# Kernel tuning notes

Measured on AMD Instinct MI355X. Metric: run time of the kernel, lower is better.

## Reference

```python
import jax, jax.numpy as jnp
import numpy as np

K_HEADS, D_HEAD = 8, 8
D = K_HEADS * D_HEAD  # 64


def _fc(x, W, b=None, relu=False):
    # 1x1 Conv2D over (B,T,N,C) == per-position dense
    y = x @ W
    if b is not None:
        y = y + b
    return jax.nn.relu(y) if relu else y


def _split_heads(x):
    # (B,T,N,K*d) -> (K,B,T,N,d); matches torch.cat(torch.split(x, d, -1), 0)
    B, T, N, _ = x.shape
    return x.reshape(B, T, N, K_HEADS, D_HEAD).transpose(3, 0, 1, 2, 4)


def _merge_heads(x):
    # (K,B,T,N,d) -> (B,T,N,K*d); matches torch.cat(torch.split(x, B, 0), -1)
    K, B, T, N, d = x.shape
    return x.transpose(1, 2, 3, 0, 4).reshape(B, T, N, K * d)


def _forward(X, TLE, key_padding_mask, *P):
    (sa_Wq, sa_bq, sa_Wk, sa_bk, sa_Wv, sa_bv, sa_Wo1, sa_bo1, sa_Wo2, sa_bo2,
     ta_Wq, ta_bq, ta_Wk, ta_bk, ta_Wv, ta_bv, ta_Wo1, ta_bo1, ta_Wo2, ta_bo2,
     g_Wxs, g_Wxt, g_bxt, g_Wh1, g_bh1, g_Wh2, g_bh2) = P
    B, T, N, _ = X.shape
    scale = 1.0 / (D_HEAD ** 0.5)
    XE = jnp.concatenate([X, TLE], axis=-1)  # (B,T,N,3D)

    # ---- Spatial attention (over nodes) ----
    q = _split_heads(_fc(XE, sa_Wq, sa_bq, True))
    k = _split_heads(_fc(XE, sa_Wk, sa_bk, True))
    v = _split_heads(_fc(XE, sa_Wv, sa_bv, True))
    s = jnp.einsum('kbtnd,kbtmd->kbtnm', q, k) * scale  # (K,B,T,N,N)
    p = jax.nn.softmax(s, axis=-1)
    HS = _merge_heads(jnp.einsum('kbtnm,kbtmd->kbtnd', p, v))
    HS = _fc(_fc(HS, sa_Wo1, sa_bo1, True), sa_Wo2, sa_bo2)

    # ---- Temporal attention (over time, causal + key padding) ----
    q = _split_heads(_fc(XE, ta_Wq, ta_bq, True))
    k = _split_heads(_fc(XE, ta_Wk, ta_bk, True))
    v = _split_heads(_fc(XE, ta_Wv, ta_bv, True))
    s = jnp.einsum('kbind,kbjnd->kbnij', q, k) * scale  # (K,B,N,T,T)
    causal = jnp.tril(jnp.ones((T, T), dtype=bool))  # (T,T)
    valid_key = jnp.arange(T)[None, :] < key_padding_mask  # (B,T)
    m = causal[None, None, None] & valid_key[None, :, None, None, :]
    s = jnp.where(m, s, -jnp.inf)
    p = jax.nn.softmax(s, axis=-1)
    HT = _merge_heads(jnp.einsum('kbnij,kbjnd->kbind', p, v))
    HT = _fc(_fc(HT, ta_Wo1, ta_bo1, True), ta_Wo2, ta_bo2)

    # ---- Gated fusion + residual ----
    z = jax.nn.sigmoid(HS @ g_Wxs + HT @ g_Wxt + g_bxt)
    H = z * HS + (1.0 - z) * HT
    H = _fc(_fc(H, g_Wh1, g_bh1, True), g_Wh2, g_bh2)
    return X + H


_PARAM_SHAPES = []
for _pre in ('sa', 'ta'):
    _PARAM_SHAPES += [(_pre + '_Wq', (3 * D, D)), (_pre + '_bq', (D,)),
                      (_pre + '_Wk', (3 * D, D)), (_pre + '_bk', (D,)),
                      (_pre + '_Wv', (3 * D, D)), (_pre + '_bv', (D,)),
                      (_pre + '_Wo1', (D, D)), (_pre + '_bo1', (D,)),
                      (_pre + '_Wo2', (D, D)), (_pre + '_bo2', (D,))]
_PARAM_SHAPES += [('g_Wxs', (D, D)), ('g_Wxt', (D, D)), ('g_bxt', (D,)),
                  ('g_Wh1', (D, D)), ('g_bh1', (D,)),
                  ('g_Wh2', (D, D)), ('g_bh2', (D,))]


def setup_inputs() -> dict:
    key = jax.random.key(0)
    ks = jax.random.split(key, 3 + len(_PARAM_SHAPES))
    B, T, N = 16, 24, 128
    inp = {
        'X': jax.random.normal(ks[0], (B, T, N, D), dtype=jnp.float32),
        'TLE': jax.random.normal(ks[1], (B, T, N, 2 * D), dtype=jnp.float32),
        'key_padding_mask': jax.random.randint(ks[2], (B, 1), 1, T + 1),
    }
    for i, (nm, shp) in enumerate(_PARAM_SHAPES):
        inp[nm] = jax.random.normal(ks[3 + i], shp, dtype=jnp.float32) * 0.05
    return inp


def reference(X, TLE, key_padding_mask,
              sa_Wq, sa_bq, sa_Wk, sa_bk, sa_Wv, sa_bv, sa_Wo1, sa_bo1, sa_Wo2, sa_bo2,
              ta_Wq, ta_bq, ta_Wk, ta_bk, ta_Wv, ta_bv, ta_Wo1, ta_bo1, ta_Wo2, ta_bo2,
              g_Wxs, g_Wxt, g_bxt, g_Wh1, g_bh1, g_Wh2, g_bh2):
    return _forward(X, TLE, key_padding_mask,
                    sa_Wq, sa_bq, sa_Wk, sa_bk, sa_Wv, sa_bv, sa_Wo1, sa_bo1, sa_Wo2, sa_bo2,
                    ta_Wq, ta_bq, ta_Wk, ta_bk, ta_Wv, ta_bv, ta_Wo1, ta_bo1, ta_Wo2, ta_bo2,
                    g_Wxs, g_Wxt, g_bxt, g_Wh1, g_bh1, g_Wh2, g_bh2)
```

## Files before the change

kernel.cpp:

```cpp
#include <hip/hip_runtime.h>
#include <math.h>

#define BB 16
#define TT 24
#define NN 128
#define DD 64
#define PTOT (BB * TT * NN)
#define P64  (PTOT * 64)

typedef __attribute__((ext_vector_type(8))) short bf16x8;
typedef __attribute__((ext_vector_type(4))) float f32x4;
typedef __attribute__((ext_vector_type(16))) float f32x16;

__device__ __forceinline__ unsigned short f2bf(float f) {
    unsigned u = __builtin_bit_cast(unsigned, f);
    u = (u + 0x7fffu + ((u >> 16) & 1u)) >> 16;
    return (unsigned short)u;
}
__device__ __forceinline__ unsigned cvt_pk_bf16(float a, float b) {
    unsigned r;
    asm("v_cvt_pk_bf16_f32 %0, %1, %2" : "=v"(r) : "v"(a), "v"(b));
    return r;
}
__device__ __forceinline__ void unpack8(uint4 u, float* f) {
    f[0] = __builtin_bit_cast(float, u.x << 16);
    f[1] = __builtin_bit_cast(float, u.x & 0xFFFF0000u);
    f[2] = __builtin_bit_cast(float, u.y << 16);
    f[3] = __builtin_bit_cast(float, u.y & 0xFFFF0000u);
    f[4] = __builtin_bit_cast(float, u.z << 16);
    f[5] = __builtin_bit_cast(float, u.z & 0xFFFF0000u);
    f[6] = __builtin_bit_cast(float, u.w << 16);
    f[7] = __builtin_bit_cast(float, u.w & 0xFFFF0000u);
}
__device__ __forceinline__ uint4 pack8(const float* f) {
    uint4 o;
    o.x = cvt_pk_bf16(f[0], f[1]);
    o.y = cvt_pk_bf16(f[2], f[3]);
    o.z = cvt_pk_bf16(f[4], f[5]);
    o.w = cvt_pk_bf16(f[6], f[7]);
    return o;
}
__device__ __forceinline__ float fast_exp2(float x) {
#if __has_builtin(__builtin_amdgcn_exp2f)
    return __builtin_amdgcn_exp2f(x);
#else
    return exp2f(x);
#endif
}
__device__ __forceinline__ f32x16 zero16() {
    f32x16 z;
    #pragma unroll
    for (int i = 0; i < 16; ++i) z[i] = 0.f;
    return z;
}

__global__ __launch_bounds__(256) void wprep_all(
    const float* __restrict__ W0, const float* __restrict__ W1,
    const float* __restrict__ W2, const float* __restrict__ W3,
    const float* __restrict__ W4, const float* __restrict__ W5,
    const float* __restrict__ E0, const float* __restrict__ E1,
    const float* __restrict__ E2, const float* __restrict__ E3,
    const float* __restrict__ E4, const float* __restrict__ E5,
    const float* __restrict__ E6, const float* __restrict__ E7,
    unsigned short* __restrict__ Wt, unsigned short* __restrict__ Wt8)
{
    const int bid = blockIdx.x;
    if (bid < 288) {
        const float* Ws[6] = {W0, W1, W2, W3, W4, W5};
        const int e = bid * 256 + threadIdx.x;
        const int j = e / 12288;
        const int r = e % 12288;
        const int k = r / 64;
        const int n = r % 64;
        Wt[j * 12288 + n * 192 + k] = f2bf(Ws[j][k * 64 + n]);
    } else {
        const float* Es[8] = {E0, E1, E2, E3, E4, E5, E6, E7};
        const int e = (bid - 288) * 256 + threadIdx.x;
        const int mat = e >> 12;
        const int r = e & 4095;
        const int k = r >> 6;
        const int n = r & 63;
        Wt8[mat * 4096 + n * 64 + k] = f2bf(Es[mat][k * 64 + n]);
    }
}

__global__ __launch_bounds__(512, 4) void fused_sattn(
    const float* __restrict__ X, const float* __restrict__ TLE,
    const unsigned short* __restrict__ Wt,
    const float* __restrict__ b0, const float* __restrict__ b1,
    const float* __restrict__ b2, const float* __restrict__ b3,
    const float* __restrict__ b4, const float* __restrict__ b5,
    unsigned short* __restrict__ qt, unsigned short* __restrict__ kt,
    unsigned short* __restrict__ vt,
    unsigned short* __restrict__ HS)
{
    __shared__ __align__(16) unsigned short xe[2][16][200];
    __shared__ __align__(16) unsigned short qq[128 * 64];
    __shared__ __align__(16) unsigned short kk[128 * 64];
    __shared__ __align__(16) unsigned short vv[128 * 64];
    const int tid = threadIdx.x;
    const long p0 = (long)blockIdx.x * 128;
    const int w = tid >> 6, l = tid & 63, quad = l >> 4, l16 = l & 15;
    const int nt = w >> 1;
    const int mg = (w & 1) * 3;

    auto stage = [&](int mt, int buf) {
        #pragma unroll
        for (int i = 0; i < 2; ++i) {
            const int idx4 = tid + i * 512;
            if (idx4 < 768) {
                const int m  = idx4 / 48;
                const int kq = idx4 % 48;
                const int k  = kq * 4;
                const long p = p0 + mt * 16 + m;
                float4 v;
                if (k < 64) v = *reinterpret_cast<const float4*>(X + p * 64 + k);
                else        v = *reinterpret_cast<const float4*>(TLE + p * 128 + (k - 64));
                uint2 u;
                u.x = cvt_pk_bf16(v.x, v.y);
                u.y = cvt_pk_bf16(v.z, v.w);
                *reinterpret_cast<uint2*>(&xe[buf][m][k]) = u;
            }
        }
    };

    bf16x8 wf[3][6];
    #pragma unroll
    for (int mi = 0; mi < 3; ++mi)
        #pragma unroll
        for (int kc = 0; kc < 6; ++kc)
            wf[mi][kc] = *reinterpret_cast<const bf16x8*>(
                &Wt[(mg + mi) * 12288 + (nt * 16 + l16) * 192 + kc * 32 + quad * 8]);

    const float* bias_p[6] = {b0, b1, b2, b3, b4, b5};
    float4 bias[3];
    #pragma unroll
    for (int mi = 0; mi < 3; ++mi)
        bias[mi] = *reinterpret_cast<const float4*>(&bias_p[mg + mi][nt * 16 + quad * 4]);

    stage(0, 0);
    __syncthreads();

    const int chBase = nt * 16 + quad * 4;
    const int chunkW = nt * 2 + (quad >> 1);
    const int chSub  = (quad & 1) * 4;
    const float cs = 0.35355339059327373f * 1.4426950408889634f;

    for (int mt = 0; mt < 8; ++mt) {
        if (mt < 7) stage(mt + 1, (mt + 1) & 1);

        bf16x8 A[6];
        #pragma unroll
        for (int kc = 0; kc < 6; ++kc)
            A[kc] = *reinterpret_cast<const bf16x8*>(
                &xe[mt & 1][l16][kc * 32 + quad * 8]);

        f32x4 acc[3];
        #pragma unroll
        for (int mi = 0; mi < 3; ++mi)
            acc[mi] = (f32x4){bias[mi].x, bias[mi].y, bias[mi].z, bias[mi].w};
        #pragma unroll
        for (int kc = 0; kc < 6; ++kc)
            #pragma unroll
            for (int mi = 0; mi < 3; ++mi)
                acc[mi] = __builtin_amdgcn_mfma_f32_16x16x32_bf16(
                    wf[mi][kc], A[kc], acc[mi], 0, 0, 0);

        const int pos = mt * 16 + l16;
        if (mg == 0) {
            const int sw = pos * 64 + ((chunkW ^ (pos & 7)) << 3) + chSub;
            uint2 uq;
            uq.x = cvt_pk_bf16(fmaxf(acc[0][0], 0.f) * cs, fmaxf(acc[0][1], 0.f) * cs);
            uq.y = cvt_pk_bf16(fmaxf(acc[0][2], 0.f) * cs, fmaxf(acc[0][3], 0.f) * cs);
            *reinterpret_cast<uint2*>(&qq[sw]) = uq;
            uint2 uk;
            uk.x = cvt_pk_bf16(fmaxf(acc[1][0], 0.f), fmaxf(acc[1][1], 0.f));
            uk.y = cvt_pk_bf16(fmaxf(acc[1][2], 0.f), fmaxf(acc[1][3], 0.f));
            *reinterpret_cast<uint2*>(&kk[sw]) = uk;
            uint2 uv;
            uv.x = cvt_pk_bf16(fmaxf(acc[2][0], 0.f), fmaxf(acc[2][1], 0.f));
            uv.y = cvt_pk_bf16(fmaxf(acc[2][2], 0.f), fmaxf(acc[2][3], 0.f));
            *reinterpret_cast<uint2*>(&vv[sw]) = uv;
        } else {
            unsigned short* dstT[3] = {qt, kt, vt};
            const long gp = (p0 + pos) * 64 + chBase;
            #pragma unroll
            for (int mi = 0; mi < 3; ++mi) {
                uint2 u;
                u.x = cvt_pk_bf16(fmaxf(acc[mi][0], 0.f), fmaxf(acc[mi][1], 0.f));
                u.y = cvt_pk_bf16(fmaxf(acc[mi][2], 0.f), fmaxf(acc[mi][3], 0.f));
                *reinterpret_cast<uint2*>(&dstT[mi][gp]) = u;
            }
        }
        __builtin_amdgcn_sched_barrier(0);
        asm volatile("s_waitcnt lgkmcnt(0)" ::: "memory");
        __builtin_amdgcn_s_barrier();
        __builtin_amdgcn_sched_barrier(0);
    }

    const int h  = w;
    const int hi = l >> 5;
    const int ln = l & 31;
    bf16x8 zf = {};
    const int swz = (h ^ (ln & 7)) << 3;

    auto pvstep = [&](f32x16& st, const bf16x8& va0, const bf16x8& va1,
                      f32x16& oacc) {
        const unsigned P0 = cvt_pk_bf16(st[0],  st[1]);
        const unsigned P1 = cvt_pk_bf16(st[2],  st[3]);
        const unsigned P2 = cvt_pk_bf16(st[4],  st[5]);
        const unsigned P3 = cvt_pk_bf16(st[6],  st[7]);
        const unsigned P4 = cvt_pk_bf16(st[8],  st[9]);
        const unsigned P5 = cvt_pk_bf16(st[10], st[11]);
        const unsigned P6 = cvt_pk_bf16(st[12], st[13]);
        const unsigned P7 = cvt_pk_bf16(st[14], st[15]);
        const unsigned V0 = __shfl_xor(hi ? P0 : P2, 32);
        const unsigned V1 = __shfl_xor(hi ? P1 : P3, 32);
        const unsigned V2 = __shfl_xor(hi ? P4 : P6, 32);
        const unsigned V3 = __shfl_xor(hi ? P5 : P7, 32);
        uint4 fe, fo;
        fe.x = hi ? V0 : P0; fe.y = hi ? V1 : P1;
        fe.z = hi ? P2 : V0; fe.w = hi ? P3 : V1;
        fo.x = hi ? V2 : P4; fo.y = hi ? V3 : P5;
        fo.z = hi ? P6 : V2; fo.w = hi ? P7 : V3;
        oacc = __builtin_amdgcn_mfma_f32_32x32x16_bf16(
            va0, __builtin_bit_cast(bf16x8, fe), oacc, 0, 0, 0);
        oacc = __builtin_amdgcn_mfma_f32_32x32x16_bf16(
            va1, __builtin_bit_cast(bf16x8, fo), oacc, 0, 0, 0);
    };

    bf16x8 kf[4];
    #pragma unroll
    for (int t = 0; t < 4; ++t)
        kf[t] = hi ? zf : *reinterpret_cast<const bf16x8*>(&kk[(t * 32 + ln) * 64 + swz]);

    bf16x8 vf[8];
    #pragma unroll
    for (int c = 0; c < 8; ++c) {
        bf16x8 f = zf;
        if (ln < 8) {
            #pragma unroll
            for (int j = 0; j < 8; ++j) {
                const int m = c * 16 + hi * 8 + j;
                f[j] = (short)vv[m * 64 + ((h ^ (m & 7)) << 3) + ln];
            }
        }
        vf[c] = f;
    }

    #pragma unroll
    for (int ntq = 0; ntq < 4; ++ntq) {
        const int qrow = ntq * 32 + ln;
        bf16x8 qf = hi ? zf : *reinterpret_cast<const bf16x8*>(&qq[qrow * 64 + swz]);

        float sum = 0.f;
        f32x16 oacc = zero16();
        #pragma unroll
        for (int t = 0; t < 4; ++t) {
            f32x16 st = zero16();
            st = __builtin_amdgcn_mfma_f32_32x32x16_bf16(kf[t], qf, st, 0, 0, 0);
            #pragma unroll
            for (int r = 0; r < 16; ++r) { st[r] = fast_exp2(st[r]); sum += st[r]; }
            pvstep(st, vf[2 * t], vf[2 * t + 1], oacc);
        }
        sum += __shfl_xor(sum, 32);

        const float inv = 1.0f / sum;
        uint2 u;
        u.x = cvt_pk_bf16(oacc[0] * inv, oacc[1] * inv);
        u.y = cvt_pk_bf16(oacc[2] * inv, oacc[3] * inv);
        *reinterpret_cast<uint2*>(&HS[(p0 + qrow) * 64 + h * 8 + hi * 4]) = u;
    }
}

__global__ __launch_bounds__(192) void tattn_kernel(
    const unsigned short* __restrict__ Q, const unsigned short* __restrict__ Kb,
    const unsigned short* __restrict__ V, const int* __restrict__ kpm,
    unsigned short* __restrict__ O)
{
    __shared__ float kk[8][TT][8];
    __shared__ float vv[8][TT][8];
    const int tid = threadIdx.x;
    const int n = blockIdx.x & (NN - 1);
    const int b = blockIdx.x >> 7;

    {
        const int hs = tid / TT;
        const int j  = tid % TT;
        const long g = (((long)(b * TT + j)) * NN + n) * 64 + hs * 8;
        uint4 ku = *reinterpret_cast<const uint4*>(&Kb[g]);
        uint4 vu = *reinterpret_cast<const uint4*>(&V[g]);
        float kf[8], vf[8];
        unpack8(ku, kf); unpack8(vu, vf);
        #pragma unroll
        for (int d = 0; d < 8; ++d) { kk[hs][j][d] = kf[d]; vv[hs][j][d] = vf[d]; }
    }

    const int h = tid / TT;
    const int i = tid % TT;
    const long qb = (((long)(b * TT + i)) * NN + n) * 64 + h * 8;
    float q[8];
    {
        uint4 qu = *reinterpret_cast<const uint4*>(&Q[qb]);
        unpack8(qu, q);
    }
    __syncthreads();

    const int kp = kpm[b];
    const float scale = 0.35355339059327373f;

    float s[TT];
    #pragma unroll
    for (int j = 0; j < TT; ++j) {
        float t = 0.0f;
        #pragma unroll
        for (int d = 0; d < 8; ++d) t = fmaf(q[d], kk[h][j][d], t);
        s[j] = (j <= i && j < kp) ? t * scale : -INFINITY;
    }
    float mx = -INFINITY;
    #pragma unroll
    for (int j = 0; j < TT; ++j) mx = fmaxf(mx, s[j]);

    float sum = 0.0f;
    float acc[8];
    #pragma unroll
    for (int d = 0; d < 8; ++d) acc[d] = 0.0f;
    #pragma unroll
    for (int j = 0; j < TT; ++j) {
        const float e = __expf(s[j] - mx);
        sum += e;
        #pragma unroll
        for (int d = 0; d < 8; ++d) acc[d] = fmaf(e, vv[h][j][d], acc[d]);
    }
    const float inv = 1.0f / sum;
    float o[8];
    #pragma unroll
    for (int d = 0; d < 8; ++d) o[d] = acc[d] * inv;
    *reinterpret_cast<uint4*>(&O[qb]) = pack8(o);
}

__global__ __launch_bounds__(256) void epi_kernel(
    const float* __restrict__ X,
    const unsigned short* __restrict__ HSb, const unsigned short* __restrict__ HTb,
    const unsigned short* __restrict__ Wt8,
    const float* __restrict__ sbo1, const float* __restrict__ sbo2,
    const float* __restrict__ tbo1, const float* __restrict__ tbo2,
    const float* __restrict__ bxt,
    const float* __restrict__ bh1, const float* __restrict__ bh2,
    float* __restrict__ out)
{
    constexpr int RS = 72;
    __shared__ __align__(16) unsigned short bufA[64][RS], bufB[64][RS];
    __shared__ __align__(16) unsigned short bufC[64][RS], bufD[64][RS];
    const int tid = threadIdx.x;
    const long p0 = (long)blockIdx.x * 64;
    const int w = tid >> 6, l = tid & 63, quad = l >> 4, l16 = l & 15;
    const int chBase = w * 16 + quad * 4;

    #pragma unroll
    for (int i = 0; i < 4; ++i) {
        const int idx = tid + i * 256;
        const int m = idx >> 4;
        const int c = (idx & 15) * 4;
        *reinterpret_cast<ushort4*>(&bufA[m][c]) =
            *reinterpret_cast<const ushort4*>(&HSb[(p0 + m) * 64 + c]);
        *reinterpret_cast<ushort4*>(&bufC[m][c]) =
            *reinterpret_cast<const ushort4*>(&HTb[(p0 + m) * 64 + c]);
    }
    __syncthreads();

    auto gemm = [&](const unsigned short (*in)[RS], int mat,
                    const float* __restrict__ bias, f32x4* accO) {
        bf16x8 af[2];
        #pragma unroll
        for (int kc = 0; kc < 2; ++kc)
            af[kc] = *reinterpret_cast<const bf16x8*>(
                &Wt8[mat * 4096 + (w * 16 + l16) * 64 + kc * 32 + quad * 8]);
        const float4 b4 = *reinterpret_cast<const float4*>(&bias[chBase]);
        #pragma unroll
        for (int pt = 0; pt < 4; ++pt) {
            f32x4 acc = (f32x4){b4.x, b4.y, b4.z, b4.w};
            #pragma unroll
            for (int kc = 0; kc < 2; ++kc) {
                bf16x8 bf = *reinterpret_cast<const bf16x8*>(
                    &in[pt * 16 + l16][kc * 32 + quad * 8]);
                acc = __builtin_amdgcn_mfma_f32_16x16x32_bf16(af[kc], bf, acc, 0, 0, 0);
            }
            accO[pt] = acc;
        }
    };

    auto writeBuf = [&](unsigned short (*dst)[RS], const f32x4* v, bool relu) {
        #pragma unroll
        for (int pt = 0; pt < 4; ++pt) {
            float a0 = v[pt][0], a1 = v[pt][1], a2 = v[pt][2], a3 = v[pt][3];
            if (relu) { a0 = fmaxf(a0, 0.f); a1 = fmaxf(a1, 0.f);
                        a2 = fmaxf(a2, 0.f); a3 = fmaxf(a3, 0.f); }
            uint2 u;
            u.x = cvt_pk_bf16(a0, a1);
            u.y = cvt_pk_bf16(a2, a3);
            *reinterpret_cast<uint2*>(&dst[pt * 16 + l16][chBase]) = u;
        }
    };

    f32x4 tS[4], tT[4], HSr[4], HTr[4];

    gemm(bufA, 0, sbo1, tS);
    gemm(bufC, 2, tbo1, tT);
    __syncthreads();
    writeBuf(bufB, tS, true);
    writeBuf(bufD, tT, true);
    __syncthreads();

    gemm(bufB, 1, sbo2, HSr);
    gemm(bufD, 3, tbo2, HTr);
    __syncthreads();
    writeBuf(bufA, HSr, false);
    writeBuf(bufC, HTr, false);
    __syncthreads();

    {
        bf16x8 afS[2], afT[2];
        #pragma unroll
        for (int kc = 0; kc < 2; ++kc) {
            afS[kc] = *reinterpret_cast<const bf16x8*>(
                &Wt8[4 * 4096 + (w * 16 + l16) * 64 + kc * 32 + quad * 8]);
            afT[kc] = *reinterpret_cast<const bf16x8*>(
                &Wt8[5 * 4096 + (w * 16 + l16) * 64 + kc * 32 + quad * 8]);
        }
        const float4 b4 = *reinterpret_cast<const float4*>(&bxt[chBase]);
        #pragma unroll
        for (int pt = 0; pt < 4; ++pt) {
            f32x4 acc = (f32x4){b4.x, b4.y, b4.z, b4.w};
            #pragma unroll
            for (int kc = 0; kc < 2; ++kc) {
                bf16x8 hsf = *reinterpret_cast<const bf16x8*>(
                    &bufA[pt * 16 + l16][kc * 32 + quad * 8]);
                acc = __builtin_amdgcn_mfma_f32_16x16x32_bf16(afS[kc], hsf, acc, 0, 0, 0);
            }
            #pragma unroll
            for (int kc = 0; kc < 2; ++kc) {
                bf16x8 htf = *reinterpret_cast<const bf16x8*>(
                    &bufC[pt * 16 + l16][kc * 32 + quad * 8]);
                acc = __builtin_amdgcn_mfma_f32_16x16x32_bf16(afT[kc], htf, acc, 0, 0, 0);
            }
            f32x4 h;
            #pragma unroll
            for (int r = 0; r < 4; ++r) {
                const float z = 1.0f / (1.0f + __expf(-acc[r]));
                h[r] = z * HSr[pt][r] + (1.0f - z) * HTr[pt][r];
            }
            tS[pt] = h;
        }
    }
    writeBuf(bufB, tS, false);
    __syncthreads();

    gemm(bufB, 6, bh1, tS);
    __syncthreads();
    writeBuf(bufA, tS, true);
    __syncthreads();

    gemm(bufA, 7, bh2, tS);
    #pragma unroll
    for (int pt = 0; pt < 4; ++pt) {
        const long pos = p0 + pt * 16 + l16;
        const float4 xv = *reinterpret_cast<const float4*>(&X[pos * 64 + chBase]);
        float4 o;
        o.x = tS[pt][0] + xv.x; o.y = tS[pt][1] + xv.y;
        o.z = tS[pt][2] + xv.z; o.w = tS[pt][3] + xv.w;
        *reinterpret_cast<float4*>(&out[pos * 64 + chBase]) = o;
    }
}

extern "C" void kernel_launch(void* const* d_in, const int* in_sizes, int n_in,
                              void* d_out, int out_size, void* d_ws, size_t ws_size,
                              hipStream_t stream) {
    const float* X   = (const float*)d_in[0];
    const float* TLE = (const float*)d_in[1];
    const int* kpm   = (const int*)d_in[2];

    const float* sa_Wq = (const float*)d_in[3];  const float* sa_bq = (const float*)d_in[4];
    const float* sa_Wk = (const float*)d_in[5];  const float* sa_bk = (const float*)d_in[6];
    const float* sa_Wv = (const float*)d_in[7];  const float* sa_bv = (const float*)d_in[8];
    const float* sa_Wo1 = (const float*)d_in[9];  const float* sa_bo1 = (const float*)d_in[10];
    const float* sa_Wo2 = (const float*)d_in[11]; const float* sa_bo2 = (const float*)d_in[12];
    const float* ta_Wq = (const float*)d_in[13]; const float* ta_bq = (const float*)d_in[14];
    const float* ta_Wk = (const float*)d_in[15]; const float* ta_bk = (const float*)d_in[16];
    const float* ta_Wv = (const float*)d_in[17]; const float* ta_bv = (const float*)d_in[18];
    const float* ta_Wo1 = (const float*)d_in[19]; const float* ta_bo1 = (const float*)d_in[20];
    const float* ta_Wo2 = (const float*)d_in[21]; const float* ta_bo2 = (const float*)d_in[22];
    const float* g_Wxs = (const float*)d_in[23];
    const float* g_Wxt = (const float*)d_in[24]; const float* g_bxt = (const float*)d_in[25];
    const float* g_Wh1 = (const float*)d_in[26]; const float* g_bh1 = (const float*)d_in[27];
    const float* g_Wh2 = (const float*)d_in[28]; const float* g_bh2 = (const float*)d_in[29];

    unsigned short* wsp = (unsigned short*)d_ws;
    unsigned short* qt  = wsp + 0L * P64;
    unsigned short* kt  = wsp + 1L * P64;
    unsigned short* vt  = wsp + 2L * P64;
    unsigned short* HSb = wsp + 3L * P64;
    unsigned short* HTb = wsp + 4L * P64;
    unsigned short* Wt  = wsp + 5L * P64;
    unsigned short* Wt8 = Wt + 6 * 12288;

    float* out = (float*)d_out;

    hipLaunchKernelGGL(wprep_all, dim3(416), dim3(256), 0, stream,
                       sa_Wq, sa_Wk, sa_Wv, ta_Wq, ta_Wk, ta_Wv,
                       sa_Wo1, sa_Wo2, ta_Wo1, ta_Wo2, g_Wxs, g_Wxt, g_Wh1, g_Wh2,
                       Wt, Wt8);

    hipLaunchKernelGGL(fused_sattn, dim3(BB * TT), dim3(512), 0, stream,
                       X, TLE, Wt,
                       sa_bq, sa_bk, sa_bv, ta_bq, ta_bk, ta_bv,
                       qt, kt, vt, HSb);

    hipLaunchKernelGGL(tattn_kernel, dim3(BB * NN), dim3(192), 0, stream,
                       qt, kt, vt, kpm, HTb);

    hipLaunchKernelGGL(epi_kernel, dim3(PTOT / 64), dim3(256), 0, stream,
                       X, HSb, HTb, Wt8,
                       sa_bo1, sa_bo2, ta_bo1, ta_bo2, g_bxt, g_bh1, g_bh2,
                       out);
}
```

Baseline: 80.74 us.

## Prefetch all input tiles into registers upfront in spatial projection kernel

Replaces the per-iteration float4 staging of X/TLE rows with a single upfront burst of uint2 loads covering all 8 row-tiles, held in registers, and fully unrolls the tile loop so each iteration only converts and writes to LDS. The aim is to expose all global-load latency at once instead of serialising a load per tile. It raises register pressure (48 extra VGPRs for the loads) and switches to narrower 8-byte loads, which could reduce occupancy or load efficiency.

```diff
diff --git a/kernel.cpp b/kernel.cpp
--- a/kernel.cpp
+++ b/kernel.cpp
@@ -104,23 +104,31 @@
     const int nt = w >> 1;
     const int mg = (w & 1) * 3;
 
-    auto stage = [&](int mt, int buf) {
-        #pragma unroll
-        for (int i = 0; i < 2; ++i) {
-            const int idx4 = tid + i * 512;
-            if (idx4 < 768) {
-                const int m  = idx4 / 48;
-                const int kq = idx4 % 48;
-                const int k  = kq * 4;
-                const long p = p0 + mt * 16 + m;
-                float4 v;
-                if (k < 64) v = *reinterpret_cast<const float4*>(X + p * 64 + k);
-                else        v = *reinterpret_cast<const float4*>(TLE + p * 128 + (k - 64));
-                uint2 u;
-                u.x = cvt_pk_bf16(v.x, v.y);
-                u.y = cvt_pk_bf16(v.z, v.w);
-                *reinterpret_cast<uint2*>(&xe[buf][m][k]) = u;
-            }
+    int mj[3], kj[3];
+    const float* srcb[3];
+    long rstride[3];
+    #pragma unroll
+    for (int j = 0; j < 3; ++j) {
+        const int f = (j * 512 + tid) * 2;
+        mj[j] = f / 192;
+        kj[j] = f % 192;
+        if (kj[j] < 64) { srcb[j] = X + (p0 + mj[j]) * 64 + kj[j];  rstride[j] = 16 * 64; }
+        else            { srcb[j] = TLE + (p0 + mj[j]) * 128 + (kj[j] - 64); rstride[j] = 16 * 128; }
+    }
+
+    uint2 ld[8][3];
+    #pragma unroll
+    for (int t = 0; t < 8; ++t)
+        #pragma unroll
+        for (int j = 0; j < 3; ++j)
+            ld[t][j] = *reinterpret_cast<const uint2*>(srcb[j] + (long)t * rstride[j]);
+
+    auto stage_write = [&](int t, int buf) {
+        #pragma unroll
+        for (int j = 0; j < 3; ++j) {
+            const float a = __builtin_bit_cast(float, ld[t][j].x);
+            const float b = __builtin_bit_cast(float, ld[t][j].y);
+            *reinterpret_cast<unsigned*>(&xe[buf][mj[j]][kj[j]]) = cvt_pk_bf16(a, b);
         }
     };
 
@@ -138,7 +146,7 @@
     for (int mi = 0; mi < 3; ++mi)
         bias[mi] = *reinterpret_cast<const float4*>(&bias_p[mg + mi][nt * 16 + quad * 4]);
 
-    stage(0, 0);
+    stage_write(0, 0);
     __syncthreads();
 
     const int chBase = nt * 16 + quad * 4;
@@ -146,8 +154,9 @@
     const int chSub  = (quad & 1) * 4;
     const float cs = 0.35355339059327373f * 1.4426950408889634f;
 
+    #pragma unroll
     for (int mt = 0; mt < 8; ++mt) {
-        if (mt < 7) stage(mt + 1, (mt + 1) & 1);
+        if (mt < 7) stage_write(mt + 1, (mt + 1) & 1);
 
         bf16x8 A[6];
         #pragma unroll
```

Result: faster. 73.35 us (-9.2%).
